# Kernel tuning notes

Hardware: AMD Instinct MI355X
Metric: run time of the kernel (lower is better)

The kernel has to match this reference:

```python
import jax, jax.numpy as jnp
import numpy as np

MAX_LEN = 256
EMBED_DIM = 256
SEQ_LEN = 256
BATCH = 2048
NUM_PEAKS = 8


def setup_inputs() -> dict:
    key = jax.random.key(0)
    k1, k2, k3 = jax.random.split(key, 3)
    x = jax.random.normal(k1, (SEQ_LEN, BATCH, EMBED_DIM), dtype=jnp.float32)
    # some positions >= SEQ_LEN are invalid and must be masked out
    peak_positions = jax.random.randint(k2, (BATCH, NUM_PEAKS), 0, 300, dtype=jnp.int64)
    table = jax.random.normal(k3, (MAX_LEN, EMBED_DIM), dtype=jnp.float32)  # nn.Embedding weight
    return {"x": x, "peak_positions": peak_positions, "table": table}


def _sinusoidal_pe(seq_len, dim, dtype):
    # NB: original uses log(1000.0), not 10000.0 -- kept faithful.
    position = jnp.arange(seq_len, dtype=jnp.float32)[:, None]            # [S, 1]
    div_term = jnp.exp(jnp.arange(0, dim, 2, dtype=jnp.float32) * (-np.log(1000.0) / dim))
    ang = position * div_term                                              # [S, D/2]
    pe = jnp.zeros((seq_len, dim), dtype=jnp.float32)
    pe = pe.at[:, 0::2].set(jnp.sin(ang)).at[:, 1::2].set(jnp.cos(ang))
    return pe.astype(dtype)


def reference(x, peak_positions, table):
    seq_len, batch, dim = x.shape
    max_len = table.shape[0]
    # positional encoding add
    pe = _sinusoidal_pe(seq_len, dim, x.dtype)                             # [S, D]
    x = x + pe[:, None, :]
    # batched masked gather-scatter (replaces the per-sample Python loop)
    valid = (peak_positions >= 0) & (peak_positions < seq_len)             # [B, P]
    # route invalid peaks to a dump row (seq_len) that is sliced off after scatter
    idx = jnp.where(valid, peak_positions, seq_len)                        # [B, P]
    emb = table[jnp.clip(peak_positions, 0, max_len - 1)]                  # [B, P, D]
    b_idx = jnp.arange(batch)[:, None]                                     # [B, 1]
    peak_embed = (
        jnp.zeros((seq_len + 1, batch, dim), dtype=x.dtype)
        .at[idx, b_idx].set(emb)[:seq_len]                                 # [S, B, D]
    )
    return x + peak_embed
```

## Files before the change

### kernel.cpp

```cpp
#include <hip/hip_runtime.h>


typedef float f32x4 __attribute__((ext_vector_type(4)));

namespace {
constexpr int S       = 256;
constexpr int Bn      = 2048;
constexpr int P       = 8;
constexpr int D4      = 64;
constexpr int BTILE   = 128;
constexpr int NBT     = Bn / BTILE;
constexpr int THREADS = 256;
constexpr int ITERS   = BTILE * D4 / THREADS;
}

__global__ __launch_bounds__(THREADS)
void pe_peak_kernel(const float* __restrict__ x,
                    const unsigned* __restrict__ pk,
                    const float* __restrict__ table,
                    float* __restrict__ out)
{
    __shared__ f32x4 s_pe[D4];
    __shared__ f32x4 s_pt[D4];
    __shared__ unsigned long long s_mb[2];
    __shared__ int s_is64;

    const int t  = threadIdx.x;
    const int s  = blockIdx.x >> 4;
    const int b0 = (blockIdx.x & (NBT - 1)) * BTILE;

    {
        unsigned hw = (t < 32) ? pk[2 * t + 1] : 0u;
        unsigned long long nz = __ballot(hw != 0u);
        if (t == 0) s_is64 = (nz == 0ull) ? 1 : 0;
    }

    if (t < D4) {
        const float c = -6.907755278982137f / 256.0f;
        float a0 = (float)s * expf((float)(4 * t) * c);
        float a1 = (float)s * expf((float)(4 * t + 2) * c);
        f32x4 pe4;
        pe4.x = sinf(a0); pe4.y = cosf(a0);
        pe4.z = sinf(a1); pe4.w = cosf(a1);
        f32x4 tb4 = reinterpret_cast<const f32x4*>(table)[s * D4 + t];
        s_pe[t] = pe4;
        s_pt[t] = pe4 + tb4;
    }
    __syncthreads();

    bool m = false;
    if (t < BTILE) {
        const int b = b0 + t;
        if (s_is64) {
            #pragma unroll
            for (int p = 0; p < P; ++p) m |= (pk[(size_t)(b * P + p) * 2] == (unsigned)s);
        } else {
            #pragma unroll
            for (int p = 0; p < P; ++p) m |= (pk[b * P + p] == (unsigned)s);
        }
    }
    {
        unsigned long long bal = __ballot(m);
        if (t < 128 && (t & 63) == 0) s_mb[t >> 6] = bal;
    }
    __syncthreads();

    const int lane = t & 63;
    const int w    = t >> 6;
    const f32x4 pe4 = s_pe[lane];
    const f32x4 pt4 = s_pt[lane];
    const unsigned long long mb0 = s_mb[0];
    const unsigned long long mb1 = s_mb[1];

    const size_t base = ((size_t)s * Bn + b0) * D4;
    const f32x4* __restrict__ xr = reinterpret_cast<const f32x4*>(x) + base;
    f32x4* __restrict__ orow     = reinterpret_cast<f32x4*>(out) + base;

    #pragma unroll
    for (int j0 = 0; j0 < ITERS; j0 += 8) {
        f32x4 v[8];
        #pragma unroll
        for (int u = 0; u < 8; ++u)
            v[u] = __builtin_nontemporal_load(xr + (size_t)(j0 + u) * THREADS + t);
        #pragma unroll
        for (int u = 0; u < 8; ++u) {
            const int j = j0 + u;
            const unsigned long long mb = (j < 16) ? mb0 : mb1;
            const bool hit = (mb >> ((4 * j + w) & 63)) & 1ull;
            const f32x4 a = hit ? pt4 : pe4;
            __builtin_nontemporal_store(v[u] + a, orow + (size_t)j * THREADS + t);
        }
    }
}

extern "C" void kernel_launch(void* const* d_in, const int* in_sizes, int n_in,
                              void* d_out, int out_size, void* d_ws, size_t ws_size,
                              hipStream_t stream) {
    const float*    x     = (const float*)d_in[0];
    const unsigned* pk    = (const unsigned*)d_in[1];
    const float*    table = (const float*)d_in[2];
    float*          out   = (float*)d_out;

    pe_peak_kernel<<<dim3(S * NBT), dim3(THREADS), 0, stream>>>(x, pk, table, out);
}
```

Measured before the change: 200.9 us.

## Split PE and peak-mask computation into a prep kernel before streaming

Adds a prep kernel that, for each sequence position, computes the sinusoidal PE row, PE plus table row, and a per-batch hit bitmask, and writes them to workspace. The streaming kernel then only loads these precomputed values and streams x to out, dropping the per-block transcendental math, peak scans, shared memory and barriers. In exchange it adds a second launch, and the prep kernel runs only 256 blocks that scan all peak positions. If the workspace is too small, the original fused kernel is used instead.

New measurement: 210.1 us. 4.6% more time.

```diff
diff --git a/kernel.cpp b/kernel.cpp
--- a/kernel.cpp
+++ b/kernel.cpp
@@ -12,13 +12,105 @@
 constexpr int NBT     = Bn / BTILE;
 constexpr int THREADS = 256;
 constexpr int ITERS   = BTILE * D4 / THREADS;
+constexpr int CHUNK   = 8;
+
+constexpr size_t WS_PE_OFF   = 0;
+constexpr size_t WS_PT_OFF   = (size_t)S * D4;
+constexpr size_t WS_MASK_OFF = (size_t)2 * S * D4 * 16;
+constexpr size_t WS_NEEDED   = WS_MASK_OFF + (size_t)S * (Bn / 64) * 8;
 }
 
 __global__ __launch_bounds__(THREADS)
-void pe_peak_kernel(const float* __restrict__ x,
-                    const unsigned* __restrict__ pk,
+void pe_prep_kernel(const unsigned* __restrict__ pk,
                     const float* __restrict__ table,
-                    float* __restrict__ out)
+                    f32x4* __restrict__ ws_pe,
+                    unsigned long long* __restrict__ ws_mask)
+{
+    const int s = blockIdx.x;
+    const int t = threadIdx.x;
+
+    __shared__ int s_is64;
+    {
+        unsigned hw = (t < 32) ? pk[2 * t + 1] : 0u;
+        unsigned long long nz = __ballot(hw != 0u);
+        if (t == 0) s_is64 = (nz == 0ull) ? 1 : 0;
+    }
+    __syncthreads();
+    const bool is64 = (s_is64 != 0);
+
+    if (t < D4) {
+        const float c = -6.907755278982137f / 256.0f;
+        float a0 = (float)s * expf((float)(4 * t) * c);
+        float a1 = (float)s * expf((float)(4 * t + 2) * c);
+        f32x4 pe4;
+        pe4.x = sinf(a0); pe4.y = cosf(a0);
+        pe4.z = sinf(a1); pe4.w = cosf(a1);
+        f32x4 tb4 = reinterpret_cast<const f32x4*>(table)[s * D4 + t];
+        ws_pe[(size_t)s * D4 + t]              = pe4;
+        ws_pe[WS_PT_OFF + (size_t)s * D4 + t]  = pe4 + tb4;
+    }
+
+    const int w = t >> 6;
+    #pragma unroll
+    for (int k = 0; k < Bn / THREADS; ++k) {
+        const int b = k * THREADS + t;
+        bool m = false;
+        if (is64) {
+            #pragma unroll
+            for (int p = 0; p < P; ++p) m |= (pk[(size_t)(b * P + p) * 2] == (unsigned)s);
+        } else {
+            #pragma unroll
+            for (int p = 0; p < P; ++p) m |= (pk[b * P + p] == (unsigned)s);
+        }
+        unsigned long long bal = __ballot(m);
+        if ((t & 63) == 0) ws_mask[(size_t)s * (Bn / 64) + k * 4 + w] = bal;
+    }
+}
+
+__global__ __launch_bounds__(THREADS)
+void pe_stream_kernel(const float* __restrict__ x,
+                      const f32x4* __restrict__ ws_pe,
+                      const unsigned long long* __restrict__ ws_mask,
+                      float* __restrict__ out)
+{
+    const int t  = threadIdx.x;
+    const int s  = blockIdx.x >> 4;
+    const int b0 = (blockIdx.x & (NBT - 1)) * BTILE;
+
+    const int lane = t & 63;
+    const int w    = t >> 6;
+
+    const f32x4 pe4 = ws_pe[(size_t)s * D4 + lane];
+    const f32x4 pt4 = ws_pe[WS_PT_OFF + (size_t)s * D4 + lane];
+    const unsigned long long mb0 = ws_mask[(size_t)s * (Bn / 64) + (b0 >> 6)];
+    const unsigned long long mb1 = ws_mask[(size_t)s * (Bn / 64) + (b0 >> 6) + 1];
+
+    const size_t base = ((size_t)s * Bn + b0) * D4;
+    const f32x4* __restrict__ xr = reinterpret_cast<const f32x4*>(x) + base;
+    f32x4* __restrict__ orow     = reinterpret_cast<f32x4*>(out) + base;
+
+    #pragma unroll
+    for (int j0 = 0; j0 < ITERS; j0 += CHUNK) {
+        f32x4 v[CHUNK];
+        #pragma unroll
+        for (int u = 0; u < CHUNK; ++u)
+            v[u] = __builtin_nontemporal_load(xr + (size_t)(j0 + u) * THREADS + t);
+        #pragma unroll
+        for (int u = 0; u < CHUNK; ++u) {
+            const int j = j0 + u;
+            const unsigned long long mb = (j < 16) ? mb0 : mb1;
+            const bool hit = (mb >> ((4 * j + w) & 63)) & 1ull;
+            const f32x4 a = hit ? pt4 : pe4;
+            __builtin_nontemporal_store(v[u] + a, orow + (size_t)j * THREADS + t);
+        }
+    }
+}
+
+__global__ __launch_bounds__(THREADS)
+void pe_peak_fused_kernel(const float* __restrict__ x,
+                          const unsigned* __restrict__ pk,
+                          const float* __restrict__ table,
+                          float* __restrict__ out)
 {
     __shared__ f32x4 s_pe[D4];
     __shared__ f32x4 s_pt[D4];
@@ -77,13 +169,13 @@
     f32x4* __restrict__ orow     = reinterpret_cast<f32x4*>(out) + base;
 
     #pragma unroll
-    for (int j0 = 0; j0 < ITERS; j0 += 8) {
-        f32x4 v[8];
-        #pragma unroll
-        for (int u = 0; u < 8; ++u)
+    for (int j0 = 0; j0 < ITERS; j0 += CHUNK) {
+        f32x4 v[CHUNK];
+        #pragma unroll
+        for (int u = 0; u < CHUNK; ++u)
             v[u] = __builtin_nontemporal_load(xr + (size_t)(j0 + u) * THREADS + t);
         #pragma unroll
-        for (int u = 0; u < 8; ++u) {
+        for (int u = 0; u < CHUNK; ++u) {
             const int j = j0 + u;
             const unsigned long long mb = (j < 16) ? mb0 : mb1;
             const bool hit = (mb >> ((4 * j + w) & 63)) & 1ull;
@@ -101,5 +193,13 @@
     const float*    table = (const float*)d_in[2];
     float*          out   = (float*)d_out;
 
-    pe_peak_kernel<<<dim3(S * NBT), dim3(THREADS), 0, stream>>>(x, pk, table, out);
-}
+    if (ws_size >= WS_NEEDED) {
+        f32x4* ws_pe = (f32x4*)d_ws;
+        unsigned long long* ws_mask =
+            (unsigned long long*)((char*)d_ws + WS_MASK_OFF);
+        pe_prep_kernel<<<dim3(S), dim3(THREADS), 0, stream>>>(pk, table, ws_pe, ws_mask);
+        pe_stream_kernel<<<dim3(S * NBT), dim3(THREADS), 0, stream>>>(x, ws_pe, ws_mask, out);
+    } else {
+        pe_peak_fused_kernel<<<dim3(S * NBT), dim3(THREADS), 0, stream>>>(x, pk, table, out);
+    }
+}
```
